# Kernel optimization log

Hardware: AMD Instinct MI355X
Metric: run time of the kernel (lower is better)

## Reference

```python
import jax, jax.numpy as jnp
import numpy as np

B, N, E, H, P = 4, 512, 512, 32, 128
D = E // H
SCALING = D ** -0.5
EPS = 1e-5


def layer_norm(x, g, b):
    mu = jnp.mean(x, axis=-1, keepdims=True)
    var = jnp.var(x, axis=-1, keepdims=True)
    return (x - mu) * jax.lax.rsqrt(var + EPS) * g + b


def setup_inputs() -> dict:
    key = jax.random.key(0)
    ks = jax.random.split(key, 12)
    inp = {
        "query": jax.random.normal(ks[0], (B, N, E), jnp.float32),
        "pair": jax.random.normal(ks[1], (B, N, N, P), jnp.float32),
        "attn_mask": jnp.zeros((B, H, N, N), jnp.float32),
        "delta_pos": jax.random.normal(ks[2], (B, N, N, 3), jnp.float32),
        # parameters
        "ln_g": jnp.ones((E,), jnp.float32),
        "ln_b": jnp.zeros((E,), jnp.float32),
        "Wq": jax.random.normal(ks[3], (E, E), jnp.float32) * (1.0 / np.sqrt(E)),
        "Wk": jax.random.normal(ks[4], (E, E), jnp.float32) * (1.0 / np.sqrt(E)),
        "Wv": jax.random.normal(ks[5], (E, E), jnp.float32) * (1.0 / np.sqrt(E)),
        "pln_g": jnp.ones((P,), jnp.float32),
        "pln_b": jnp.zeros((P,), jnp.float32),
        "Wb": jax.random.normal(ks[6], (H, P), jnp.float32) * (1.0 / np.sqrt(P)),
        "bb": jnp.zeros((H,), jnp.float32),
        "Wf": jax.random.normal(ks[7], (1, E), jnp.float32) * (1.0 / np.sqrt(E)),
    }
    return inp


def reference(query, pair, attn_mask, delta_pos,
              ln_g, ln_b, Wq, Wk, Wv, pln_g, pln_b, Wb, bb, Wf):
    x = layer_norm(query, ln_g, ln_b)                       # (B,N,E)
    q = (x @ Wq.T).reshape(B, N, H, D).transpose(0, 2, 1, 3) * SCALING  # (B,H,N,D)
    k = (x @ Wk.T).reshape(B, N, H, D).transpose(0, 2, 1, 3)
    v = (x @ Wv.T).reshape(B, N, H, D).transpose(0, 2, 1, 3)
    attn = jnp.einsum('bhid,bhjd->bhij', q, k)              # (B,H,N,N)
    pair_n = layer_norm(pair, pln_g, pln_b)
    bias = (pair_n @ Wb.T + bb).transpose(0, 3, 1, 2)       # (B,H,N,N)
    attn = jax.nn.softmax(attn + bias + attn_mask, axis=-1)  # dropout off (eval)
    # rot_attn_probs: attn (B,H,N,N) * delta_pos (B,N,N,3) -> contract over j with v
    # out per (b, i, coord c, head h, d): sum_j attn[b,h,i,j]*delta_pos[b,i,j,c]*v[b,h,j,d]
    xo = jnp.einsum('bhij,bijc,bhjd->bichd', attn, delta_pos, v)  # (B,N,3,H,D)
    xo = xo.reshape(B, N, 3, E)
    cur_force = (xo @ Wf.T).reshape(B, N, 3)
    return cur_force
```

## Files before the change

### kernel.cpp

```cpp
#include <hip/hip_runtime.h>
#include <hip/hip_bf16.h>
#include <stdint.h>

constexpr int cB = 4, cN = 512, cE = 512, cH = 32, cP = 128;

typedef __attribute__((ext_vector_type(8))) short bf16x8;
typedef __attribute__((ext_vector_type(4))) float f32x4;

__device__ __forceinline__ unsigned short f2bf(float f) {
    union { float f; unsigned u; } v; v.f = f;
    unsigned u = v.u;
    u += 0x7fffu + ((u >> 16) & 1u);
    return (unsigned short)(u >> 16);
}
__device__ __forceinline__ float bf2f(unsigned short s) {
    union { unsigned u; float f; } v; v.u = ((unsigned)s) << 16;
    return v.f;
}

__global__ __launch_bounds__(256) void ln_query_kernel(
    const float* __restrict__ q, const float* __restrict__ g,
    const float* __restrict__ b, float* __restrict__ xn)
{
    int row = blockIdx.x;
    int t = threadIdx.x;
    const float* xr = q + (size_t)row * cE;
    float2 v = *(const float2*)(xr + t * 2);
    float s = v.x + v.y;
    float ss = v.x * v.x + v.y * v.y;
    #pragma unroll
    for (int o = 32; o > 0; o >>= 1) {
        s  += __shfl_down(s, o, 64);
        ss += __shfl_down(ss, o, 64);
    }
    __shared__ float red[8];
    int wv = t >> 6, ln = t & 63;
    if (ln == 0) { red[wv] = s; red[wv + 4] = ss; }
    __syncthreads();
    if (t == 0) {
        float S = red[0] + red[1] + red[2] + red[3];
        float SS = red[4] + red[5] + red[6] + red[7];
        float mu = S * (1.0f / cE);
        float var = SS * (1.0f / cE) - mu * mu;
        red[0] = mu; red[1] = rsqrtf(var + 1e-5f);
    }
    __syncthreads();
    float mu = red[0], rs = red[1];
    float2 gg = *(const float2*)(g + t * 2);
    float2 bb2 = *(const float2*)(b + t * 2);
    float2 o2;
    o2.x = (v.x - mu) * rs * gg.x + bb2.x;
    o2.y = (v.y - mu) * rs * gg.y + bb2.y;
    *(float2*)(xn + (size_t)row * cE + t * 2) = o2;
}

__global__ void setup_kernel(
    const float* __restrict__ Wb, const float* __restrict__ pg,
    const float* __restrict__ pb, const float* __restrict__ bbv,
    unsigned short* __restrict__ Wbp, float* __restrict__ Sh,
    float* __restrict__ cbh)
{
    int h = threadIdx.x;
    if (h < cH) {
        float s = 0.f, c = bbv[h];
        for (int p = 0; p < cP; ++p) {
            float wv = Wb[h * cP + p];
            float wp = wv * pg[p];
            s += wp;
            c += pb[p] * wv;
            Wbp[h * cP + p] = f2bf(wp);
        }
        Sh[h] = s; cbh[h] = c;
    }
}

__global__ __launch_bounds__(64) void qkv_kernel(
    const float* __restrict__ xn,
    const float* __restrict__ Wq, const float* __restrict__ Wk,
    const float* __restrict__ Wv, const float* __restrict__ Wf,
    float* __restrict__ Q, float* __restrict__ K, float* __restrict__ w)
{
    int mtile = blockIdx.x & 31;
    int ntile = blockIdx.x >> 5;
    int mat = ntile >> 3;
    int ncol0 = (ntile & 7) * 64;
    const float* W = (mat == 0) ? Wq : ((mat == 1) ? Wk : Wv);
    int rm = mtile * 64;
    int t = threadIdx.x;
    int tm = t >> 3, tn = t & 7;

    __shared__ float As[32][68];
    __shared__ float Bs[32][68];
    float acc[8][8];
    #pragma unroll
    for (int i = 0; i < 8; ++i)
        #pragma unroll
        for (int j = 0; j < 8; ++j) acc[i][j] = 0.f;

    for (int k0 = 0; k0 < cE; k0 += 32) {
        #pragma unroll
        for (int s = 0; s < 8; ++s) {
            int f = t + 64 * s;
            int row = f >> 3, kq = f & 7;
            float4 v = *(const float4*)(xn + (size_t)(rm + row) * cE + k0 + kq * 4);
            As[kq * 4 + 0][row] = v.x; As[kq * 4 + 1][row] = v.y;
            As[kq * 4 + 2][row] = v.z; As[kq * 4 + 3][row] = v.w;
            float4 u = *(const float4*)(W + (size_t)(ncol0 + row) * cE + k0 + kq * 4);
            Bs[kq * 4 + 0][row] = u.x; Bs[kq * 4 + 1][row] = u.y;
            Bs[kq * 4 + 2][row] = u.z; Bs[kq * 4 + 3][row] = u.w;
        }
        __syncthreads();
        #pragma unroll
        for (int kk = 0; kk < 32; ++kk) {
            float a[8], bv[8];
            #pragma unroll
            for (int i = 0; i < 8; ++i) a[i] = As[kk][tm * 8 + i];
            #pragma unroll
            for (int j = 0; j < 8; ++j) bv[j] = Bs[kk][tn * 8 + j];
            #pragma unroll
            for (int i = 0; i < 8; ++i)
                #pragma unroll
                for (int j = 0; j < 8; ++j) acc[i][j] = fmaf(a[i], bv[j], acc[i][j]);
        }
        __syncthreads();
    }

    if (mat < 2) {
        float scale = (mat == 0) ? 0.25f : 1.0f;
        float* dst = (mat == 0) ? Q : K;
        #pragma unroll
        for (int i = 0; i < 8; ++i) {
            int r = rm + tm * 8 + i;
            #pragma unroll
            for (int j = 0; j < 8; ++j)
                dst[(size_t)r * cE + ncol0 + tn * 8 + j] = acc[i][j] * scale;
        }
    } else {
        int col0 = ncol0 + tn * 8;
        int h = col0 >> 4;
        float wf[8];
        #pragma unroll
        for (int j = 0; j < 8; ++j) wf[j] = Wf[col0 + j];
        #pragma unroll
        for (int i = 0; i < 8; ++i) {
            int r = rm + tm * 8 + i;
            float part = 0.f;
            #pragma unroll
            for (int j = 0; j < 8; ++j) part = fmaf(acc[i][j], wf[j], part);
            atomicAdd(&w[(size_t)r * cH + h], part);
        }
    }
}

__global__ __launch_bounds__(256) void attn_kernel(
    const float* __restrict__ pair, const float* __restrict__ mask,
    const float* __restrict__ dpos, const float* __restrict__ Q,
    const float* __restrict__ K, const float* __restrict__ w,
    const unsigned short* __restrict__ Wbp, const float* __restrict__ Sh_g,
    const float* __restrict__ cb_g, float* __restrict__ out)
{
    int bi = blockIdx.x;
    int b = bi >> 9, i = bi & 511;
    int t = threadIdx.x;
    int lane = t & 63, wv = t >> 6;

    __shared__ __align__(16) unsigned short Ap[64 * 136];
    __shared__ __align__(16) unsigned short Bw[32 * 136];
    __shared__ float biasT[64][33];
    __shared__ float qrow[512];
    __shared__ float mrow[64], rrow[64];
    __shared__ float mt[64][33];
    __shared__ float dl[64][4];
    __shared__ float Shs[32], cbs[32];
    __shared__ float statred[64][8];

    {
        const ushort4* src = (const ushort4*)Wbp;
        #pragma unroll
        for (int s = 0; s < 4; ++s) {
            int f = t + 256 * s;
            int hh = f >> 5, p4 = f & 31;
            ushort4 v = src[f];
            *(ushort4*)&Bw[hh * 136 + p4 * 4] = v;
        }
    }
    if (t < 128) {
        float4 qv = *(const float4*)(Q + (size_t)bi * cE + t * 4);
        *(float4*)&qrow[t * 4] = qv;
    }
    if (t < 32) { Shs[t] = Sh_g[t]; cbs[t] = cb_g[t]; }
    __syncthreads();

    int h = t & 31, js = t >> 5;
    float qreg[16];
    #pragma unroll
    for (int d = 0; d < 16; ++d) qreg[d] = qrow[h * 16 + d];
    float Sh_loc = Shs[h], cb_loc = cbs[h];

    float m = -1e30f, l = 0.f, a0 = 0.f, a1 = 0.f, a2 = 0.f;

    const float* pbase = pair + (size_t)bi * cN * cP;
    const float* dbase = dpos + (size_t)bi * cN * 3;
    const float* Kbase = K + (size_t)b * cN * cE;
    const float* wbase = w + (size_t)b * cN * cH;

    for (int j0 = 0; j0 < cN; j0 += 64) {
        #pragma unroll
        for (int s = 0; s < 8; ++s) {
            int f = t + 256 * s;
            int row = f >> 5, c4 = f & 31;
            float4 v = *(const float4*)(pbase + (size_t)(j0 + row) * cP + c4 * 4);
            ushort4 u;
            u.x = f2bf(v.x); u.y = f2bf(v.y); u.z = f2bf(v.z); u.w = f2bf(v.w);
            *(ushort4*)&Ap[row * 136 + c4 * 4] = u;
        }
        #pragma unroll
        for (int s = 0; s < 2; ++s) {
            int f = t + 256 * s;
            int hh = f >> 4, c4 = f & 15;
            float4 v = *(const float4*)(mask + ((size_t)(b * cH + hh) * cN + i) * cN + j0 + c4 * 4);
            mt[c4 * 4 + 0][hh] = v.x; mt[c4 * 4 + 1][hh] = v.y;
            mt[c4 * 4 + 2][hh] = v.z; mt[c4 * 4 + 3][hh] = v.w;
        }
        if (t < 64) {
            const float* dp = dbase + (size_t)(j0 + t) * 3;
            dl[t][0] = dp[0]; dl[t][1] = dp[1]; dl[t][2] = dp[2];
        }
        __syncthreads();

        {
            int r = t >> 2, q = t & 3;
            float s1 = 0.f, s2 = 0.f;
            #pragma unroll
            for (int p = 0; p < 32; ++p) {
                float f = bf2f(Ap[r * 136 + q * 32 + p]);
                s1 += f; s2 = fmaf(f, f, s2);
            }
            statred[r][q] = s1; statred[r][q + 4] = s2;
        }
        __syncthreads();
        if (t < 64) {
            float s1 = statred[t][0] + statred[t][1] + statred[t][2] + statred[t][3];
            float s2 = statred[t][4] + statred[t][5] + statred[t][6] + statred[t][7];
            float mu = s1 * (1.0f / cP);
            float var = s2 * (1.0f / cP) - mu * mu;
            mrow[t] = mu;
            rrow[t] = rsqrtf(var + 1e-5f);
        }
        __syncthreads();

        {
            f32x4 acc0 = {0.f, 0.f, 0.f, 0.f}, acc1 = {0.f, 0.f, 0.f, 0.f};
            int arow = wv * 16 + (lane & 15);
            int kq = (lane >> 4) * 8;
            #pragma unroll
            for (int kb = 0; kb < 4; ++kb) {
                int k = kb * 32 + kq;
                bf16x8 af = *(const bf16x8*)&Ap[arow * 136 + k];
                bf16x8 b0 = *(const bf16x8*)&Bw[(lane & 15) * 136 + k];
                bf16x8 b1 = *(const bf16x8*)&Bw[(16 + (lane & 15)) * 136 + k];
                acc0 = __builtin_amdgcn_mfma_f32_16x16x32_bf16(af, b0, acc0, 0, 0, 0);
                acc1 = __builtin_amdgcn_mfma_f32_16x16x32_bf16(af, b1, acc1, 0, 0, 0);
            }
            int crow = wv * 16 + (lane >> 4) * 4;
            int ccol = lane & 15;
            #pragma unroll
            for (int r = 0; r < 4; ++r) {
                biasT[crow + r][ccol] = acc0[r];
                biasT[crow + r][16 + ccol] = acc1[r];
            }
        }
        __syncthreads();

        #pragma unroll
        for (int jj = 0; jj < 8; ++jj) {
            int jr = js * 8 + jj;
            int j = j0 + jr;
            float bias = rrow[jr] * (biasT[jr][h] - mrow[jr] * Sh_loc) + cb_loc;
            const float4* kp4 = (const float4*)(Kbase + (size_t)j * cE + h * 16);
            float qk = 0.f;
            #pragma unroll
            for (int d4 = 0; d4 < 4; ++d4) {
                float4 kv = kp4[d4];
                qk = fmaf(qreg[d4 * 4 + 0], kv.x, qk);
                qk = fmaf(qreg[d4 * 4 + 1], kv.y, qk);
                qk = fmaf(qreg[d4 * 4 + 2], kv.z, qk);
                qk = fmaf(qreg[d4 * 4 + 3], kv.w, qk);
            }
            float z = qk + bias + mt[jr][h];
            float wj = wbase[(size_t)j * cH + h];
            float mn = fmaxf(m, z);
            float sc = __expf(m - mn);
            float p = __expf(z - mn);
            l = l * sc + p;
            float pw = p * wj;
            a0 = fmaf(pw, dl[jr][0], a0 * sc);
            a1 = fmaf(pw, dl[jr][1], a1 * sc);
            a2 = fmaf(pw, dl[jr][2], a2 * sc);
            m = mn;
        }
        __syncthreads();
    }

    float* red = (float*)mt;
    red[(h * 8 + js) * 6 + 0] = m;
    red[(h * 8 + js) * 6 + 1] = l;
    red[(h * 8 + js) * 6 + 2] = a0;
    red[(h * 8 + js) * 6 + 3] = a1;
    red[(h * 8 + js) * 6 + 4] = a2;
    __syncthreads();
    for (int s = 4; s >= 1; s >>= 1) {
        if (js < s) {
            float* p1 = &red[(h * 8 + js) * 6];
            float* p2 = &red[(h * 8 + js + s) * 6];
            float m1 = p1[0], m2 = p2[0];
            float mn = fmaxf(m1, m2);
            float s1 = __expf(m1 - mn), s2 = __expf(m2 - mn);
            p1[0] = mn;
            p1[1] = p1[1] * s1 + p2[1] * s2;
            p1[2] = p1[2] * s1 + p2[2] * s2;
            p1[3] = p1[3] * s1 + p2[3] * s2;
            p1[4] = p1[4] * s1 + p2[4] * s2;
        }
        __syncthreads();
    }
    if (js == 0) {
        float linv = 1.0f / red[h * 48 + 1];
        biasT[h][0] = red[h * 48 + 2] * linv;
        biasT[h][1] = red[h * 48 + 3] * linv;
        biasT[h][2] = red[h * 48 + 4] * linv;
    }
    __syncthreads();
    if (t < 3) {
        float s = 0.f;
        #pragma unroll
        for (int hh = 0; hh < cH; ++hh) s += biasT[hh][t];
        out[(size_t)bi * 3 + t] = s;
    }
}

extern "C" void kernel_launch(void* const* d_in, const int* in_sizes, int n_in,
                              void* d_out, int out_size, void* d_ws, size_t ws_size,
                              hipStream_t stream)
{
    const float* query = (const float*)d_in[0];
    const float* pair  = (const float*)d_in[1];
    const float* amask = (const float*)d_in[2];
    const float* dpos  = (const float*)d_in[3];
    const float* ln_g  = (const float*)d_in[4];
    const float* ln_b  = (const float*)d_in[5];
    const float* Wq    = (const float*)d_in[6];
    const float* Wk    = (const float*)d_in[7];
    const float* Wv    = (const float*)d_in[8];
    const float* pg    = (const float*)d_in[9];
    const float* pb    = (const float*)d_in[10];
    const float* Wb    = (const float*)d_in[11];
    const float* bbv   = (const float*)d_in[12];
    const float* Wf    = (const float*)d_in[13];
    float* out = (float*)d_out;

    char* ws = (char*)d_ws;
    float* xn = (float*)ws;
    float* Q  = (float*)(ws + (size_t)4 * 1048576);
    float* K  = (float*)(ws + (size_t)8 * 1048576);
    float* w  = (float*)(ws + (size_t)12 * 1048576);
    unsigned short* Wbp = (unsigned short*)(ws + (size_t)12 * 1048576 + 262144);
    float* Sh  = (float*)(ws + (size_t)12 * 1048576 + 262144 + 8192);
    float* cbh = (float*)(ws + (size_t)12 * 1048576 + 262144 + 8192 + 128);

    ln_query_kernel<<<cB * cN, 256, 0, stream>>>(query, ln_g, ln_b, xn);
    setup_kernel<<<1, 64, 0, stream>>>(Wb, pg, pb, bbv, Wbp, Sh, cbh);
    hipMemsetAsync(w, 0, (size_t)cB * cN * cH * sizeof(float), stream);
    qkv_kernel<<<32 * 24, 64, 0, stream>>>(xn, Wq, Wk, Wv, Wf, Q, K, w);
    attn_kernel<<<cB * cN, 256, 0, stream>>>(pair, amask, dpos, Q, K, w, Wbp, Sh, cbh, out);
}
```

Before: 962.1 us.

## Prefetch pair tiles into registers and restructure attention loop barriers

The attention kernel now loads the next 64-row pair tile and delta_pos slice into registers while the current tile is processed, double-buffers delta_pos in shared memory, reads the mask directly per thread instead of transposing it through shared memory, and merges the row-stat reduction into fewer barriers. Q and per-head constants are loaded straight into registers, and launch bounds request four blocks per CU. The QKV GEMM moves from 64 threads with 8x8 tiles to 256 threads with 4x4 tiles and float4 stores. The register prefetch raises register pressure, which may work against the requested occupancy.

```diff
diff --git a/kernel.cpp b/kernel.cpp
--- a/kernel.cpp
+++ b/kernel.cpp
@@ -74,7 +74,7 @@
     }
 }
 
-__global__ __launch_bounds__(64) void qkv_kernel(
+__global__ __launch_bounds__(256) void qkv_kernel(
     const float* __restrict__ xn,
     const float* __restrict__ Wq, const float* __restrict__ Wk,
     const float* __restrict__ Wv, const float* __restrict__ Wf,
@@ -87,20 +87,20 @@
     const float* W = (mat == 0) ? Wq : ((mat == 1) ? Wk : Wv);
     int rm = mtile * 64;
     int t = threadIdx.x;
-    int tm = t >> 3, tn = t & 7;
+    int tm = t >> 4, tn = t & 15;
 
     __shared__ float As[32][68];
     __shared__ float Bs[32][68];
-    float acc[8][8];
+    float acc[4][4];
     #pragma unroll
-    for (int i = 0; i < 8; ++i)
-        #pragma unroll
-        for (int j = 0; j < 8; ++j) acc[i][j] = 0.f;
+    for (int i = 0; i < 4; ++i)
+        #pragma unroll
+        for (int j = 0; j < 4; ++j) acc[i][j] = 0.f;
 
     for (int k0 = 0; k0 < cE; k0 += 32) {
         #pragma unroll
-        for (int s = 0; s < 8; ++s) {
-            int f = t + 64 * s;
+        for (int s = 0; s < 2; ++s) {
+            int f = t + 256 * s;
             int row = f >> 3, kq = f & 7;
             float4 v = *(const float4*)(xn + (size_t)(rm + row) * cE + k0 + kq * 4);
             As[kq * 4 + 0][row] = v.x; As[kq * 4 + 1][row] = v.y;
@@ -112,15 +112,15 @@
         __syncthreads();
         #pragma unroll
         for (int kk = 0; kk < 32; ++kk) {
-            float a[8], bv[8];
-            #pragma unroll
-            for (int i = 0; i < 8; ++i) a[i] = As[kk][tm * 8 + i];
-            #pragma unroll
-            for (int j = 0; j < 8; ++j) bv[j] = Bs[kk][tn * 8 + j];
-            #pragma unroll
-            for (int i = 0; i < 8; ++i)
+            float a[4], bv[4];
+            #pragma unroll
+            for (int i = 0; i < 4; ++i) a[i] = As[kk][tm * 4 + i];
+            #pragma unroll
+            for (int j = 0; j < 4; ++j) bv[j] = Bs[kk][tn * 4 + j];
+            #pragma unroll
+            for (int i = 0; i < 4; ++i)
                 #pragma unroll
-                for (int j = 0; j < 8; ++j) acc[i][j] = fmaf(a[i], bv[j], acc[i][j]);
+                for (int j = 0; j < 4; ++j) acc[i][j] = fmaf(a[i], bv[j], acc[i][j]);
         }
         __syncthreads();
     }
@@ -129,30 +129,31 @@
         float scale = (mat == 0) ? 0.25f : 1.0f;
         float* dst = (mat == 0) ? Q : K;
         #pragma unroll
-        for (int i = 0; i < 8; ++i) {
-            int r = rm + tm * 8 + i;
-            #pragma unroll
-            for (int j = 0; j < 8; ++j)
-                dst[(size_t)r * cE + ncol0 + tn * 8 + j] = acc[i][j] * scale;
+        for (int i = 0; i < 4; ++i) {
+            int r = rm + tm * 4 + i;
+            float4 o;
+            o.x = acc[i][0] * scale; o.y = acc[i][1] * scale;
+            o.z = acc[i][2] * scale; o.w = acc[i][3] * scale;
+            *(float4*)(dst + (size_t)r * cE + ncol0 + tn * 4) = o;
         }
     } else {
-        int col0 = ncol0 + tn * 8;
+        int col0 = ncol0 + tn * 4;
         int h = col0 >> 4;
-        float wf[8];
-        #pragma unroll
-        for (int j = 0; j < 8; ++j) wf[j] = Wf[col0 + j];
-        #pragma unroll
-        for (int i = 0; i < 8; ++i) {
-            int r = rm + tm * 8 + i;
+        float wf[4];
+        #pragma unroll
+        for (int j = 0; j < 4; ++j) wf[j] = Wf[col0 + j];
+        #pragma unroll
+        for (int i = 0; i < 4; ++i) {
+            int r = rm + tm * 4 + i;
             float part = 0.f;
             #pragma unroll
-            for (int j = 0; j < 8; ++j) part = fmaf(acc[i][j], wf[j], part);
+            for (int j = 0; j < 4; ++j) part = fmaf(acc[i][j], wf[j], part);
             atomicAdd(&w[(size_t)r * cH + h], part);
         }
     }
 }
 
-__global__ __launch_bounds__(256) void attn_kernel(
+__global__ __launch_bounds__(256, 4) void attn_kernel(
     const float* __restrict__ pair, const float* __restrict__ mask,
     const float* __restrict__ dpos, const float* __restrict__ Q,
     const float* __restrict__ K, const float* __restrict__ w,
@@ -166,12 +167,9 @@
 
     __shared__ __align__(16) unsigned short Ap[64 * 136];
     __shared__ __align__(16) unsigned short Bw[32 * 136];
-    __shared__ float biasT[64][33];
-    __shared__ float qrow[512];
+    __shared__ float biasT[64 * 33];
     __shared__ float mrow[64], rrow[64];
-    __shared__ float mt[64][33];
-    __shared__ float dl[64][4];
-    __shared__ float Shs[32], cbs[32];
+    __shared__ __align__(16) float dl2[2][192];
     __shared__ float statred[64][8];
 
     {
@@ -184,18 +182,21 @@
             *(ushort4*)&Bw[hh * 136 + p4 * 4] = v;
         }
     }
-    if (t < 128) {
-        float4 qv = *(const float4*)(Q + (size_t)bi * cE + t * 4);
-        *(float4*)&qrow[t * 4] = qv;
-    }
-    if (t < 32) { Shs[t] = Sh_g[t]; cbs[t] = cb_g[t]; }
-    __syncthreads();
 
     int h = t & 31, js = t >> 5;
+    int g = js, c4 = t & 31;
+
     float qreg[16];
-    #pragma unroll
-    for (int d = 0; d < 16; ++d) qreg[d] = qrow[h * 16 + d];
-    float Sh_loc = Shs[h], cb_loc = cbs[h];
+    {
+        const float4* qp = (const float4*)(Q + (size_t)bi * cE + h * 16);
+        #pragma unroll
+        for (int d4 = 0; d4 < 4; ++d4) {
+            float4 qv = qp[d4];
+            qreg[d4 * 4 + 0] = qv.x; qreg[d4 * 4 + 1] = qv.y;
+            qreg[d4 * 4 + 2] = qv.z; qreg[d4 * 4 + 3] = qv.w;
+        }
+    }
+    float Sh_loc = Sh_g[h], cb_loc = cb_g[h];
 
     float m = -1e30f, l = 0.f, a0 = 0.f, a1 = 0.f, a2 = 0.f;
 
@@ -203,29 +204,44 @@
     const float* dbase = dpos + (size_t)bi * cN * 3;
     const float* Kbase = K + (size_t)b * cN * cE;
     const float* wbase = w + (size_t)b * cN * cH;
-
-    for (int j0 = 0; j0 < cN; j0 += 64) {
+    const float* mbase = mask + ((size_t)(b * cH + h) * cN + i) * cN;
+
+    float4 pf[8];
+    #pragma unroll
+    for (int s = 0; s < 8; ++s)
+        pf[s] = *(const float4*)(pbase + (size_t)(g + 8 * s) * cP + c4 * 4);
+    float4 dpf = {0.f, 0.f, 0.f, 0.f};
+    if (t < 48) dpf = *(const float4*)(dbase + t * 4);
+
+    for (int it = 0; it < 8; ++it) {
+        int j0 = it * 64;
+        int buf = it & 1;
+
         #pragma unroll
         for (int s = 0; s < 8; ++s) {
-            int f = t + 256 * s;
-            int row = f >> 5, c4 = f & 31;
-            float4 v = *(const float4*)(pbase + (size_t)(j0 + row) * cP + c4 * 4);
             ushort4 u;
-            u.x = f2bf(v.x); u.y = f2bf(v.y); u.z = f2bf(v.z); u.w = f2bf(v.w);
-            *(ushort4*)&Ap[row * 136 + c4 * 4] = u;
-        }
-        #pragma unroll
-        for (int s = 0; s < 2; ++s) {
-            int f = t + 256 * s;
-            int hh = f >> 4, c4 = f & 15;
-            float4 v = *(const float4*)(mask + ((size_t)(b * cH + hh) * cN + i) * cN + j0 + c4 * 4);
-            mt[c4 * 4 + 0][hh] = v.x; mt[c4 * 4 + 1][hh] = v.y;
-            mt[c4 * 4 + 2][hh] = v.z; mt[c4 * 4 + 3][hh] = v.w;
-        }
-        if (t < 64) {
-            const float* dp = dbase + (size_t)(j0 + t) * 3;
-            dl[t][0] = dp[0]; dl[t][1] = dp[1]; dl[t][2] = dp[2];
-        }
+            u.x = f2bf(pf[s].x); u.y = f2bf(pf[s].y);
+            u.z = f2bf(pf[s].z); u.w = f2bf(pf[s].w);
+            *(ushort4*)&Ap[(g + 8 * s) * 136 + c4 * 4] = u;
+        }
+        if (t < 48) *(float4*)&dl2[buf][t * 4] = dpf;
+
+        if (it < 7) {
+            const float* pb2 = pbase + (size_t)(j0 + 64) * cP;
+            #pragma unroll
+            for (int s = 0; s < 8; ++s)
+                pf[s] = *(const float4*)(pb2 + (size_t)(g + 8 * s) * cP + c4 * 4);
+            if (t < 48) dpf = *(const float4*)(dbase + (size_t)(j0 + 64) * 3 + t * 4);
+        }
+
+        float mka[8];
+        {
+            float4 mf0 = *(const float4*)(mbase + j0 + js * 8);
+            float4 mf1 = *(const float4*)(mbase + j0 + js * 8 + 4);
+            mka[0] = mf0.x; mka[1] = mf0.y; mka[2] = mf0.z; mka[3] = mf0.w;
+            mka[4] = mf1.x; mka[5] = mf1.y; mka[6] = mf1.z; mka[7] = mf1.w;
+        }
+
         __syncthreads();
 
         {
@@ -238,16 +254,6 @@
             }
             statred[r][q] = s1; statred[r][q + 4] = s2;
         }
-        __syncthreads();
-        if (t < 64) {
-            float s1 = statred[t][0] + statred[t][1] + statred[t][2] + statred[t][3];
-            float s2 = statred[t][4] + statred[t][5] + statred[t][6] + statred[t][7];
-            float mu = s1 * (1.0f / cP);
-            float var = s2 * (1.0f / cP) - mu * mu;
-            mrow[t] = mu;
-            rrow[t] = rsqrtf(var + 1e-5f);
-        }
-        __syncthreads();
 
         {
             f32x4 acc0 = {0.f, 0.f, 0.f, 0.f}, acc1 = {0.f, 0.f, 0.f, 0.f};
@@ -266,9 +272,19 @@
             int ccol = lane & 15;
             #pragma unroll
             for (int r = 0; r < 4; ++r) {
-                biasT[crow + r][ccol] = acc0[r];
-                biasT[crow + r][16 + ccol] = acc1[r];
+                biasT[(crow + r) * 33 + ccol] = acc0[r];
+                biasT[(crow + r) * 33 + 16 + ccol] = acc1[r];
             }
+        }
+        __syncthreads();
+
+        if (t < 64) {
+            float s1 = statred[t][0] + statred[t][1] + statred[t][2] + statred[t][3];
+            float s2 = statred[t][4] + statred[t][5] + statred[t][6] + statred[t][7];
+            float mu = s1 * (1.0f / cP);
+            float var = s2 * (1.0f / cP) - mu * mu;
+            mrow[t] = mu;
+            rrow[t] = rsqrtf(var + 1e-5f);
         }
         __syncthreads();
 
@@ -276,7 +292,7 @@
         for (int jj = 0; jj < 8; ++jj) {
             int jr = js * 8 + jj;
             int j = j0 + jr;
-            float bias = rrow[jr] * (biasT[jr][h] - mrow[jr] * Sh_loc) + cb_loc;
+            float bias = rrow[jr] * (biasT[jr * 33 + h] - mrow[jr] * Sh_loc) + cb_loc;
             const float4* kp4 = (const float4*)(Kbase + (size_t)j * cE + h * 16);
             float qk = 0.f;
             #pragma unroll
@@ -287,22 +303,22 @@
                 qk = fmaf(qreg[d4 * 4 + 2], kv.z, qk);
                 qk = fmaf(qreg[d4 * 4 + 3], kv.w, qk);
             }
-            float z = qk + bias + mt[jr][h];
+            float z = qk + bias + mka[jj];
             float wj = wbase[(size_t)j * cH + h];
             float mn = fmaxf(m, z);
             float sc = __expf(m - mn);
             float p = __expf(z - mn);
             l = l * sc + p;
             float pw = p * wj;
-            a0 = fmaf(pw, dl[jr][0], a0 * sc);
-            a1 = fmaf(pw, dl[jr][1], a1 * sc);
-            a2 = fmaf(pw, dl[jr][2], a2 * sc);
+            a0 = fmaf(pw, dl2[buf][jr * 3 + 0], a0 * sc);
+            a1 = fmaf(pw, dl2[buf][jr * 3 + 1], a1 * sc);
+            a2 = fmaf(pw, dl2[buf][jr * 3 + 2], a2 * sc);
             m = mn;
         }
-        __syncthreads();
-    }
-
-    float* red = (float*)mt;
+    }
+
+    __syncthreads();
+    float* red = biasT;
     red[(h * 8 + js) * 6 + 0] = m;
     red[(h * 8 + js) * 6 + 1] = l;
     red[(h * 8 + js) * 6 + 2] = a0;
@@ -326,15 +342,15 @@
     }
     if (js == 0) {
         float linv = 1.0f / red[h * 48 + 1];
-        biasT[h][0] = red[h * 48 + 2] * linv;
-        biasT[h][1] = red[h * 48 + 3] * linv;
-        biasT[h][2] = red[h * 48 + 4] * linv;
+        biasT[1536 + h * 3 + 0] = red[h * 48 + 2] * linv;
+        biasT[1536 + h * 3 + 1] = red[h * 48 + 3] * linv;
+        biasT[1536 + h * 3 + 2] = red[h * 48 + 4] * linv;
     }
     __syncthreads();
     if (t < 3) {
         float s = 0.f;
         #pragma unroll
-        for (int hh = 0; hh < cH; ++hh) s += biasT[hh][t];
+        for (int hh = 0; hh < cH; ++hh) s += biasT[1536 + hh * 3 + t];
         out[(size_t)bi * 3 + t] = s;
     }
 }
@@ -371,6 +387,6 @@
     ln_query_kernel<<<cB * cN, 256, 0, stream>>>(query, ln_g, ln_b, xn);
     setup_kernel<<<1, 64, 0, stream>>>(Wb, pg, pb, bbv, Wbp, Sh, cbh);
     hipMemsetAsync(w, 0, (size_t)cB * cN * cH * sizeof(float), stream);
-    qkv_kernel<<<32 * 24, 64, 0, stream>>>(xn, Wq, Wk, Wv, Wf, Q, K, w);
+    qkv_kernel<<<32 * 24, 256, 0, stream>>>(xn, Wq, Wk, Wv, Wf, Q, K, w);
     attn_kernel<<<cB * cN, 256, 0, stream>>>(pair, amask, dpos, Q, K, w, Wbp, Sh, cbh, out);
 }
```

Measured after the change: 1.012 ms. +5.2%, slower.
